# Kernel tuning notes

Measured on AMD Instinct MI355X. Metric: run time of the kernel, lower is better.

## Reference

```python
import jax, jax.numpy as jnp
import numpy as np

NUM_HEADS = 8
ROPE_BASE = 10000.0


def _rope(x):
    # x: [b, n, c]; RoPE with channel_dims=(n,), feature_dim=c, k_max=c//2
    b, n, c = x.shape
    k_max = c // 2
    theta = 1.0 / (ROPE_BASE ** (jnp.arange(k_max, dtype=jnp.float32) / k_max))
    angles = jnp.arange(n, dtype=jnp.float32)[:, None] * theta  # [n, k_max]
    cos = jnp.cos(angles)
    sin = jnp.sin(angles)
    xr = x[..., 0::2]  # real parts  [b, n, k_max]
    xi = x[..., 1::2]  # imag parts
    pr = cos * xr - sin * xi
    pi = cos * xi + sin * xr
    # original concatenates real half then imag half (no re-interleave)
    return jnp.concatenate([pr, pi], axis=-1)


def setup_inputs() -> dict:
    key = jax.random.key(0)
    ks = jax.random.split(key, 5)
    b, n, c = 4, 4096, 1024
    x = jax.random.normal(ks[0], (b, n, c), dtype=jnp.float32)
    qk_w = jax.random.normal(ks[1], (c, 2 * c), dtype=jnp.float32) * (1.0 / np.sqrt(c))
    qk_b = jnp.zeros((2 * c,), dtype=jnp.float32)
    lepe_w = jax.random.normal(ks[2], (3, c, c), dtype=jnp.float32) * (1.0 / np.sqrt(3 * c))  # [W, I, O]
    lepe_b = jnp.zeros((c,), dtype=jnp.float32)
    return {"x": x, "qk_w": qk_w, "qk_b": qk_b, "lepe_w": lepe_w, "lepe_b": lepe_b}


def reference(x, qk_w, qk_b, lepe_w, lepe_b):
    b, n, c = x.shape
    h = NUM_HEADS
    d = c // h

    qk = x @ qk_w + qk_b
    q, k = jnp.split(qk, 2, axis=-1)
    q = jax.nn.elu(q) + 1.0
    k = jax.nn.elu(k) + 1.0

    q_rope = _rope(q)
    k_rope = _rope(k)

    def to_heads(t):  # [b, n, c] -> [b, h, n, d]
        return t.reshape(b, n, h, d).transpose(0, 2, 1, 3)

    qh = to_heads(q)
    kh = to_heads(k)
    qr = to_heads(q_rope)
    kr = to_heads(k_rope)
    vh = to_heads(x)

    # z = 1 / (q . mean_n(k) + eps)  -> [b, h, n, 1]
    k_mean = jnp.mean(kh, axis=2, keepdims=True)  # [b, h, 1, d]
    z = 1.0 / (jnp.einsum('bhnd,bhmd->bhnm', qh, k_mean) + 1e-6)

    # kv = k_rope^T v / sqrt(n)  -> [b, h, d, d]
    kv = jnp.einsum('bhnd,bhne->bhde', kr, vh) * (1.0 / jnp.sqrt(jnp.float32(n)))
    out = jnp.einsum('bhnd,bhde->bhne', qr, kv) * z  # [b, h, n, d]

    out = out.transpose(0, 2, 1, 3).reshape(b, n, c)

    # lepe: Conv1D(dim, 3, padding='same') applied to v (== original x)
    lepe = jax.lax.conv_general_dilated(
        x, lepe_w, window_strides=(1,), padding='SAME',
        dimension_numbers=('NWC', 'WIO', 'NWC')) + lepe_b
    return out + lepe
```

## Files before the change

kernel.cpp:

```cpp
#include <hip/hip_runtime.h>
#include <cmath>

#define BB 4
#define NN 4096
#define CC 1024
#define HH 8
#define DD 128
#define MM (BB*NN)
#define NP (NN+2)

typedef __attribute__((ext_vector_type(8))) short bf16x8;
typedef __attribute__((ext_vector_type(4))) float f32x4;

static __device__ __forceinline__ unsigned short f2bf(float f) {
    unsigned int u = __float_as_uint(f);
    unsigned int r = (u + 0x7FFF + ((u >> 16) & 1)) >> 16;
    return (unsigned short)r;
}
static __device__ __forceinline__ float bf2f(short s) {
    return __uint_as_float(((unsigned int)(unsigned short)s) << 16);
}
static __device__ __forceinline__ float4 bf4(ushort4 u) {
    float4 f;
    f.x = __uint_as_float((unsigned int)u.x << 16);
    f.y = __uint_as_float((unsigned int)u.y << 16);
    f.z = __uint_as_float((unsigned int)u.z << 16);
    f.w = __uint_as_float((unsigned int)u.w << 16);
    return f;
}

static __device__ __forceinline__ void load_lds16(const void* g, void* l) {
    __builtin_amdgcn_global_load_lds(
        (const __attribute__((address_space(1))) unsigned int*)g,
        (__attribute__((address_space(3))) unsigned int*)l, 16, 0, 0);
}

static __device__ __forceinline__ int swz(int row, int ko) {
    return (row * 64 + ko) ^ ((row & 7) << 3);
}

#define CFENCE() asm volatile("" ::: "memory")
#define BAR() do { CFENCE(); __builtin_amdgcn_s_barrier(); CFENCE(); } while (0)

__global__ __launch_bounds__(256) void padx_kernel(
    const float* __restrict__ x, unsigned short* __restrict__ xpad)
{
    const int r = blockIdx.x;
    const int b = r / NP, p = r % NP;
    const int c = threadIdx.x * 4;
    ushort4 v = {0, 0, 0, 0};
    if (p >= 1 && p <= NN) {
        const float4 f = *(const float4*)&x[(size_t)(b * NN + p - 1) * CC + c];
        v.x = f2bf(f.x); v.y = f2bf(f.y); v.z = f2bf(f.z); v.w = f2bf(f.w);
    }
    *(ushort4*)&xpad[(size_t)r * CC + c] = v;
}

__global__ __launch_bounds__(256) void transpose_bf16_kernel(
    const float* __restrict__ src, unsigned short* __restrict__ dst,
    int R, int Cc)
{
    __shared__ float t[32][33];
    const int r0 = blockIdx.y * 32, c0 = blockIdx.x * 32;
    const int tx = threadIdx.x & 31, ty = threadIdx.x >> 5;
    #pragma unroll
    for (int i = 0; i < 4; ++i) {
        int r = ty + i * 8;
        t[r][tx] = src[(size_t)(r0 + r) * Cc + c0 + tx];
    }
    __syncthreads();
    #pragma unroll
    for (int i = 0; i < 4; ++i) {
        int r = ty + i * 8;
        dst[(size_t)(c0 + r) * R + r0 + tx] = f2bf(t[tx][r]);
    }
}

static __device__ __forceinline__ void stage_half(
    const unsigned short* __restrict__ g, int stride,
    unsigned short* lds, int tid)
{
    const int wb = tid & ~63;
    #pragma unroll
    for (int l = 0; l < 2; ++l) {
        const int c = l * 512 + tid;
        const int row = c >> 3;
        const int col8 = (c & 7) ^ (row & 7);
        load_lds16(&g[(size_t)row * stride + col8 * 8],
                   &lds[(size_t)(l * 512 + wb) * 8]);
    }
}

static __device__ __forceinline__ void lda4(
    const unsigned short* __restrict__ h, int lr0, int rl, int ko, bf16x8* o)
{
    #pragma unroll
    for (int i = 0; i < 4; ++i)
        o[i] = *(const bf16x8*)&h[swz(lr0 + i * 16 + rl, ko)];
}

static __device__ __forceinline__ void mfma_quad(
    f32x4 (*acc)[4], int mfb, const bf16x8* af, const bf16x8* bfr)
{
    __builtin_amdgcn_s_setprio(1);
    #pragma unroll
    for (int i = 0; i < 4; ++i)
        #pragma unroll
        for (int nf = 0; nf < 4; ++nf)
            acc[mfb + i][nf] = __builtin_amdgcn_mfma_f32_16x16x32_bf16(
                af[i], bfr[nf], acc[mfb + i][nf], 0, 0, 0);
    __builtin_amdgcn_s_setprio(0);
}

#define KTILE_4PHASE(Ah, Bh, blr0, STAGE_A0, STAGE_A1, STAGE_B0, STAGE_B1, HAVE_NEXT) \
    do {                                                                     \
        bf16x8 af_[4], af2_[4], bfr_[4], bfr2_[4];                           \
                                                                \
        if (HAVE_NEXT) {                                                     \
            STAGE_A0;                                                        \
            asm volatile("s_waitcnt vmcnt(2)" ::: "memory");                 \
        } else {                                                             \
            asm volatile("s_waitcnt vmcnt(0)" ::: "memory");                 \
        }                                                                    \
        BAR();                                                               \
        lda4(Ah, 0, rl, ko0, af_);                                           \
        lda4(Bh, blr0, rl, ko0, bfr_);                                       \
        mfma_quad(acc, 0, af_, bfr_);                                        \
        BAR();                                                               \
                                                                \
        lda4(Ah, 64, rl, ko0, af2_);                                         \
        if (HAVE_NEXT) { STAGE_A1; }                                         \
        BAR();                                                               \
        mfma_quad(acc, 4, af2_, bfr_);                                       \
        BAR();                                                               \
                                                                \
        lda4(Ah, 0, rl, ko1, af_);                                           \
        lda4(Bh, blr0, rl, ko1, bfr2_);                                      \
        if (HAVE_NEXT) { STAGE_B0; }                                         \
        BAR();                                                               \
        mfma_quad(acc, 0, af_, bfr2_);                                       \
        BAR();                                                               \
                                                                \
        lda4(Ah, 64, rl, ko1, af2_);                                         \
        if (HAVE_NEXT) { STAGE_B1; }                                         \
        BAR();                                                               \
        mfma_quad(acc, 4, af2_, bfr2_);                                      \
        BAR();                                                               \
    } while (0)

__global__ __launch_bounds__(512) void gemm_qk_mfma(
    const unsigned short* __restrict__ xpad, const unsigned short* __restrict__ wT,
    const float* __restrict__ bias, unsigned short* __restrict__ qbuf,
    unsigned short* __restrict__ kbuf, float* __restrict__ ksum)
{
    __shared__ __align__(16) unsigned short SA[2][2][8192];
    __shared__ __align__(16) unsigned short SB[2][2][8192];
    const int m0 = blockIdx.x * 256;
    const int n0 = blockIdx.y * 256;
    const int tid = threadIdx.x;
    const int lane = tid & 63;
    const int wv = tid >> 6;
    const int wr = wv >> 2, wc = wv & 3;
    const int b = m0 >> 12;
    const int rbase = m0 + 1 + 2 * b;
    const int rl = lane & 15;
    const int ko0 = (lane >> 4) * 8;
    const int ko1 = 32 + ko0;
    const int blr0 = (wc & 1) * 64;

    const unsigned short* Agl = &xpad[(size_t)rbase * CC];
    const unsigned short* Bgl = &wT[(size_t)n0 * CC];

    f32x4 acc[8][4] = {};
    stage_half(Agl, CC, SA[0][0], tid);
    stage_half(&Agl[(size_t)128 * CC], CC, SA[0][1], tid);
    stage_half(Bgl, CC, SB[0][0], tid);
    stage_half(&Bgl[(size_t)128 * CC], CC, SB[0][1], tid);

    const int NT = 16;
    for (int t = 0; t < NT; ++t) {
        const int cur = t & 1;
        const unsigned short* Ah = SA[cur][wr];
        const unsigned short* Bh = SB[cur][wc >> 1];
        const int k1 = (t + 1) * 64;
        KTILE_4PHASE(Ah, Bh, blr0,
            stage_half(&Agl[k1], CC, SA[cur ^ 1][0], tid),
            stage_half(&Agl[(size_t)128 * CC + k1], CC, SA[cur ^ 1][1], tid),
            stage_half(&Bgl[k1], CC, SB[cur ^ 1][0], tid),
            stage_half(&Bgl[(size_t)128 * CC + k1], CC, SB[cur ^ 1][1], tid),
            (t + 1 < NT));
    }

    const bool khalf = (n0 >= CC);
    const int col = lane & 15, rb4 = (lane >> 4) * 4;
    #pragma unroll
    for (int nf = 0; nf < 4; ++nf) {
        const int n = n0 + wc * 64 + nf * 16 + col;
        const float bn = bias[n];
        float csum = 0.0f;
        #pragma unroll
        for (int mf = 0; mf < 8; ++mf)
            #pragma unroll
            for (int r = 0; r < 4; ++r) {
                const int m = m0 + wr * 128 + mf * 16 + rb4 + r;
                float v = acc[mf][nf][r] + bn;
                v = (v > 0.0f) ? (v + 1.0f) : __expf(v);
                csum += v;
                if (!khalf) qbuf[(size_t)m * CC + n] = f2bf(v);
                else        kbuf[(size_t)m * CC + (n - CC)] = f2bf(v);
            }
        if (khalf) atomicAdd(&ksum[b * CC + (n - CC)], csum);
    }
}

__global__ __launch_bounds__(256) void rope_z_kernel(
    unsigned short* __restrict__ qbuf, const unsigned short* __restrict__ kbuf,
    const float* __restrict__ ksum, unsigned short* __restrict__ krP,
    float* __restrict__ zbuf)
{
    const int tid = threadIdx.x;
    const int row = tid >> 3;
    const int h = tid & 7;
    const int m = blockIdx.x * 32 + row;
    const int b = m >> 12;
    const int pos = m & (NN - 1);
    unsigned short* qrow = qbuf + (size_t)m * CC + h * DD;
    const unsigned short* krow = kbuf + (size_t)m * CC + h * DD;

    bf16x8 qv[16], kv8[16];
    #pragma unroll
    for (int i = 0; i < 16; ++i) {
        qv[i]  = *(const bf16x8*)&qrow[i * 8];
        kv8[i] = *(const bf16x8*)&krow[i * 8];
    }
    const float* km = ksum + b * CC + h * DD;
    float dot = 0.0f;
    #pragma unroll
    for (int i = 0; i < 16; ++i)
        #pragma unroll
        for (int jq = 0; jq < 8; ++jq)
            dot = fmaf(bf2f(qv[i][jq]), km[i * 8 + jq], dot);
    dot *= (1.0f / (float)NN);
    __syncthreads();
    zbuf[(size_t)m * HH + h] = 1.0f / (dot + 1e-6f);

    #pragma unroll
    for (int c8 = 0; c8 < 8; ++c8) {
        bf16x8 qpr, qpi, kpr, kpi;
        #pragma unroll
        for (int u = 0; u < 8; ++u) {
            const int jj = c8 * 8 + u;
            const int j = h * 64 + jj;
            const float theta = __builtin_exp2f((float)j * (-13.287712379549449f / 512.0f));
            float sv, cv;
            __sincosf((float)pos * theta, &sv, &cv);
            const int li = c8 * 2 + (u >> 2);
            const int le = (2 * u) & 7;
            const float q0 = bf2f(qv[li][le]),  q1 = bf2f(qv[li][le + 1]);
            const float k0 = bf2f(kv8[li][le]), k1 = bf2f(kv8[li][le + 1]);
            qpr[u] = (short)f2bf(cv * q0 - sv * q1);
            qpi[u] = (short)f2bf(cv * q1 + sv * q0);
            kpr[u] = (short)f2bf(cv * k0 - sv * k1);
            kpi[u] = (short)f2bf(cv * k1 + sv * k0);
        }
        *(bf16x8*)&qbuf[(size_t)m * CC + h * 64 + c8 * 8] = qpr;
        *(bf16x8*)&qbuf[(size_t)m * CC + 512 + h * 64 + c8 * 8] = qpi;
        unsigned short* kp1 = &krP[((size_t)(b * 8 + (h >> 1)) * NN + pos) * DD + (h & 1) * 64 + c8 * 8];
        unsigned short* kp2 = &krP[((size_t)(b * 8 + 4 + (h >> 1)) * NN + pos) * DD + (h & 1) * 64 + c8 * 8];
        *(bf16x8*)kp1 = kpr;
        *(bf16x8*)kp2 = kpi;
    }
}

__global__ __launch_bounds__(256) void kv_kernel(
    const unsigned short* __restrict__ krP, const unsigned short* __restrict__ xpad,
    float* __restrict__ kvpart)
{
    __shared__ float ksm[8][132];
    __shared__ float vsm[8][132];
    const int bh = blockIdx.x;
    const int slice = blockIdx.y;
    const int b = bh >> 3, h = bh & 7;
    const int n0 = slice * 256;
    const int tid = threadIdx.x;
    const int td = (tid >> 4) * 8;
    const int te = (tid & 15) * 8;
    const unsigned short* kp = krP + ((size_t)bh * NN + n0) * DD;
    const unsigned short* vp = xpad + ((size_t)(b * NP) + 1 + n0) * CC + h * DD;
    const int sr = tid >> 5;
    const int sc = (tid & 31) * 4;
    float acc[8][8] = {};
    ushort4 kq = *(const ushort4*)&kp[(size_t)sr * DD + sc];
    ushort4 vq = *(const ushort4*)&vp[(size_t)sr * CC + sc];
    for (int r0 = 0; r0 < 256; r0 += 8) {
        *(float4*)&ksm[sr][sc] = bf4(kq);
        *(float4*)&vsm[sr][sc] = bf4(vq);
        __syncthreads();
        if (r0 + 8 < 256) {
            kq = *(const ushort4*)&kp[(size_t)(r0 + 8 + sr) * DD + sc];
            vq = *(const ushort4*)&vp[(size_t)(r0 + 8 + sr) * CC + sc];
        }
        #pragma unroll
        for (int r = 0; r < 8; ++r) {
            float a[8], bv[8];
            *(float4*)&a[0]  = *(const float4*)&ksm[r][td];
            *(float4*)&a[4]  = *(const float4*)&ksm[r][td + 4];
            *(float4*)&bv[0] = *(const float4*)&vsm[r][te];
            *(float4*)&bv[4] = *(const float4*)&vsm[r][te + 4];
            #pragma unroll
            for (int i = 0; i < 8; ++i)
                #pragma unroll
                for (int j = 0; j < 8; ++j)
                    acc[i][j] = fmaf(a[i], bv[j], acc[i][j]);
        }
        __syncthreads();
    }
    float* op = kvpart + ((size_t)slice * 32 + bh) * (DD * DD);
    #pragma unroll
    for (int i = 0; i < 8; ++i)
        #pragma unroll
        for (int j = 0; j < 8; j += 4)
            *(float4*)&op[(td + i) * DD + te + j] = *(float4*)&acc[i][j];
}

__global__ __launch_bounds__(256) void kv_reduce_t_kernel(
    const float* __restrict__ kvpart, unsigned short* __restrict__ kvT)
{
    __shared__ float t[32][33];
    const int bh = blockIdx.y;
    const int dblk = blockIdx.x >> 2, eblk = blockIdx.x & 3;
    const int tx = threadIdx.x & 31, ty = threadIdx.x >> 5;
    #pragma unroll
    for (int i = 0; i < 4; ++i) {
        const int d = dblk * 32 + ty + i * 8;
        float s = 0.0f;
        #pragma unroll
        for (int sl = 0; sl < 16; ++sl)
            s += kvpart[((size_t)sl * 32 + bh) * (DD * DD) + (size_t)d * DD + eblk * 32 + tx];
        t[ty + i * 8][tx] = s * (1.0f / 64.0f);
    }
    __syncthreads();
    #pragma unroll
    for (int i = 0; i < 4; ++i) {
        const int e = ty + i * 8;
        kvT[((size_t)bh * DD + eblk * 32 + e) * DD + dblk * 32 + tx] = f2bf(t[tx][e]);
    }
}

__global__ __launch_bounds__(512) void lepe_mfma(
    const unsigned short* __restrict__ xpad, const unsigned short* __restrict__ wT,
    const float* __restrict__ bias, const unsigned short* __restrict__ qr,
    const unsigned short* __restrict__ kvT, const float* __restrict__ z,
    float* __restrict__ out)
{
    __shared__ __align__(16) unsigned short SA[2][2][8192];
    __shared__ __align__(16) unsigned short SB[2][2][8192];
    const int m0 = blockIdx.x * 256;
    const int n0 = blockIdx.y * 256;
    const int tid = threadIdx.x;
    const int lane = tid & 63;
    const int wv = tid >> 6;
    const int wr = wv >> 2, wc = wv & 3;
    const int b = m0 >> 12;
    const int rbase = m0 + 1 + 2 * b;
    const int rl = lane & 15;
    const int ko0 = (lane >> 4) * 8;
    const int ko1 = 32 + ko0;
    const int blr0 = (wc & 1) * 64;
    const int rb4 = (lane >> 4) * 4;
    const int h0 = n0 >> 7;
    const int hw = h0 + (wc >> 1);

    f32x4 acc[8][4] = {};

    #pragma unroll
    for (int kt = 0; kt < 2; ++kt) {
        stage_half(&qr[(size_t)m0 * CC + h0 * DD + kt * 64], CC, SA[0][0], tid);
        stage_half(&qr[(size_t)(m0 + 128) * CC + h0 * DD + kt * 64], CC, SA[0][1], tid);
        stage_half(&qr[(size_t)m0 * CC + (h0 + 1) * DD + kt * 64], CC, SA[1][0], tid);
        stage_half(&qr[(size_t)(m0 + 128) * CC + (h0 + 1) * DD + kt * 64], CC, SA[1][1], tid);
        stage_half(&kvT[(size_t)(b * 8 + h0) * DD * DD + kt * 64], DD, SB[0][0], tid);
        stage_half(&kvT[(size_t)(b * 8 + h0) * DD * DD + (size_t)128 * DD + kt * 64], DD, SB[0][1], tid);
        __syncthreads();
        const unsigned short* Ah = SA[wc >> 1][wr];
        const unsigned short* Bh = SB[0][wc >> 1];
        bf16x8 af[4], af2[4], bfr[4], bfr2[4];
        lda4(Ah, 0, rl, ko0, af);
        lda4(Bh, blr0, rl, ko0, bfr);
        mfma_quad(acc, 0, af, bfr);
        lda4(Ah, 64, rl, ko0, af2);
        mfma_quad(acc, 4, af2, bfr);
        lda4(Ah, 0, rl, ko1, af);
        lda4(Bh, blr0, rl, ko1, bfr2);
        mfma_quad(acc, 0, af, bfr2);
        lda4(Ah, 64, rl, ko1, af2);
        mfma_quad(acc, 4, af2, bfr2);
        __syncthreads();
    }

    #pragma unroll
    for (int mf = 0; mf < 8; ++mf)
        #pragma unroll
        for (int r = 0; r < 4; ++r) {
            const float zz = z[(size_t)(m0 + wr * 128 + mf * 16 + rb4 + r) * HH + hw];
            #pragma unroll
            for (int nf = 0; nf < 4; ++nf)
                acc[mf][nf][r] *= zz;
        }
    asm volatile("s_waitcnt vmcnt(0)" ::: "memory");

    const unsigned short* Bgl = &wT[(size_t)n0 * (3 * CC)];
    {
        const unsigned short* A0 = &xpad[(size_t)(rbase - 1) * CC];
        stage_half(A0, CC, SA[0][0], tid);
        stage_half(&A0[(size_t)128 * CC], CC, SA[0][1], tid);
        stage_half(Bgl, 3 * CC, SB[0][0], tid);
        stage_half(&Bgl[(size_t)128 * (3 * CC)], 3 * CC, SB[0][1], tid);
    }
    const int NT = 48;
    for (int t = 0; t < NT; ++t) {
        const int cur = t & 1;
        const unsigned short* Ah = SA[cur][wr];
        const unsigned short* Bh = SB[cur][wc >> 1];
        const int k1 = (t + 1) * 64;
        const int sh1 = (k1 >> 10) - 1;
        const int i1 = k1 & (CC - 1);
        const unsigned short* An = &xpad[(size_t)(rbase + sh1) * CC + i1];
        KTILE_4PHASE(Ah, Bh, blr0,
            stage_half(An, CC, SA[cur ^ 1][0], tid),
            stage_half(&An[(size_t)128 * CC], CC, SA[cur ^ 1][1], tid),
            stage_half(&Bgl[k1], 3 * CC, SB[cur ^ 1][0], tid),
            stage_half(&Bgl[(size_t)128 * (3 * CC) + k1], 3 * CC, SB[cur ^ 1][1], tid),
            (t + 1 < NT));
    }

    const int col = lane & 15;
    #pragma unroll
    for (int nf = 0; nf < 4; ++nf) {
        const int n = n0 + wc * 64 + nf * 16 + col;
        const float bn = bias[n];
        #pragma unroll
        for (int mf = 0; mf < 8; ++mf)
            #pragma unroll
            for (int r = 0; r < 4; ++r) {
                const int m = m0 + wr * 128 + mf * 16 + rb4 + r;
                out[(size_t)m * CC + n] = acc[mf][nf][r] + bn;
            }
    }
}

extern "C" void kernel_launch(void* const* d_in, const int* in_sizes, int n_in,
                              void* d_out, int out_size, void* d_ws, size_t ws_size,
                              hipStream_t stream)
{
    const float* x      = (const float*)d_in[0];
    const float* qk_w   = (const float*)d_in[1];
    const float* qk_b   = (const float*)d_in[2];
    const float* lepe_w = (const float*)d_in[3];
    const float* lepe_b = (const float*)d_in[4];
    float* out = (float*)d_out;

    float* ws     = (float*)d_ws;
    float* zbuf   = ws;
    float* ksum   = zbuf + (size_t)MM * HH;
    float* kvpart = ksum + (size_t)BB * CC;
    unsigned short* xpad = (unsigned short*)(kvpart + (size_t)16 * 32 * DD * DD);
    unsigned short* wqT  = xpad + (size_t)BB * NP * CC;
    unsigned short* wlT  = wqT + (size_t)2 * CC * CC;
    unsigned short* qbuf = wlT + (size_t)CC * 3 * CC;
    unsigned short* kbuf = qbuf + (size_t)MM * CC;
    unsigned short* krP  = kbuf + (size_t)MM * CC;
    unsigned short* kvT  = krP + (size_t)32 * NN * DD;

    hipMemsetAsync(ksum, 0, BB * CC * sizeof(float), stream);

    padx_kernel          <<<BB * NP,                      256, 0, stream>>>(x, xpad);
    transpose_bf16_kernel<<<dim3(2 * CC / 32, CC / 32),   256, 0, stream>>>(qk_w, wqT, CC, 2 * CC);
    transpose_bf16_kernel<<<dim3(CC / 32, 3 * CC / 32),   256, 0, stream>>>(lepe_w, wlT, 3 * CC, CC);

    gemm_qk_mfma      <<<dim3(MM / 256, 2048 / 256), 512, 0, stream>>>(xpad, wqT, qk_b, qbuf, kbuf, ksum);
    rope_z_kernel     <<<MM / 32,                    256, 0, stream>>>(qbuf, kbuf, ksum, krP, zbuf);
    kv_kernel         <<<dim3(32, 16),               256, 0, stream>>>(krP, xpad, kvpart);
    kv_reduce_t_kernel<<<dim3(16, 32),               256, 0, stream>>>(kvpart, kvT);
    lepe_mfma         <<<dim3(MM / 256, CC / 256),   512, 0, stream>>>(xpad, wlT, lepe_b, qbuf, kvT, zbuf, out);
}
```

Before: 521.0 us.

## Fuse RoPE into QK GEMM epilogue and simplify k-tile MFMA schedule

Applies the RoPE rotation in the QK GEMM epilogue, using a lane shuffle to fetch the paired element. Rotated q goes to a new buffer and rotated k goes straight to the permuted krP layout, so rope_z_kernel shrinks to a z-only kernel and no longer reads and rewrites q and k. The k-tile loop also replaces the four-phase barrier schedule with one staging step followed by a single mfma_ktile call, cutting barriers per tile. The costs are strided scalar bf16 stores and a sincos per element in the epilogue, plus less overlap between global staging and MFMA work.

```diff
diff --git a/kernel.cpp b/kernel.cpp
--- a/kernel.cpp
+++ b/kernel.cpp
@@ -112,10 +112,31 @@
     __builtin_amdgcn_s_setprio(0);
 }
 
+static __device__ __forceinline__ void mfma_ktile(
+    const unsigned short* __restrict__ Ah, const unsigned short* __restrict__ Bh,
+    int blr0, int rl, int kq, f32x4 acc[8][4])
+{
+    __builtin_amdgcn_s_setprio(1);
+    #pragma unroll
+    for (int ks = 0; ks < 2; ++ks) {
+        const int ko = ks * 32 + kq;
+        bf16x8 af[8], bfr[4];
+        lda4(Ah, 0, rl, ko, af);
+        lda4(Ah, 64, rl, ko, af + 4);
+        lda4(Bh, blr0, rl, ko, bfr);
+        #pragma unroll
+        for (int mf = 0; mf < 8; ++mf)
+            #pragma unroll
+            for (int nf = 0; nf < 4; ++nf)
+                acc[mf][nf] = __builtin_amdgcn_mfma_f32_16x16x32_bf16(
+                    af[mf], bfr[nf], acc[mf][nf], 0, 0, 0);
+    }
+    __builtin_amdgcn_s_setprio(0);
+}
+
 #define KTILE_4PHASE(Ah, Bh, blr0, STAGE_A0, STAGE_A1, STAGE_B0, STAGE_B1, HAVE_NEXT) \
     do {                                                                     \
         bf16x8 af_[4], af2_[4], bfr_[4], bfr2_[4];                           \
-                                                                \
         if (HAVE_NEXT) {                                                     \
             STAGE_A0;                                                        \
             asm volatile("s_waitcnt vmcnt(2)" ::: "memory");                 \
@@ -127,20 +148,17 @@
         lda4(Bh, blr0, rl, ko0, bfr_);                                       \
         mfma_quad(acc, 0, af_, bfr_);                                        \
         BAR();                                                               \
-                                                                \
         lda4(Ah, 64, rl, ko0, af2_);                                         \
         if (HAVE_NEXT) { STAGE_A1; }                                         \
         BAR();                                                               \
         mfma_quad(acc, 4, af2_, bfr_);                                       \
         BAR();                                                               \
-                                                                \
         lda4(Ah, 0, rl, ko1, af_);                                           \
         lda4(Bh, blr0, rl, ko1, bfr2_);                                      \
         if (HAVE_NEXT) { STAGE_B0; }                                         \
         BAR();                                                               \
         mfma_quad(acc, 0, af_, bfr2_);                                       \
         BAR();                                                               \
-                                                                \
         lda4(Ah, 64, rl, ko1, af2_);                                         \
         if (HAVE_NEXT) { STAGE_B1; }                                         \
         BAR();                                                               \
@@ -151,7 +169,8 @@
 __global__ __launch_bounds__(512) void gemm_qk_mfma(
     const unsigned short* __restrict__ xpad, const unsigned short* __restrict__ wT,
     const float* __restrict__ bias, unsigned short* __restrict__ qbuf,
-    unsigned short* __restrict__ kbuf, float* __restrict__ ksum)
+    unsigned short* __restrict__ qrbuf, unsigned short* __restrict__ krP,
+    float* __restrict__ ksum)
 {
     __shared__ __align__(16) unsigned short SA[2][2][8192];
     __shared__ __align__(16) unsigned short SB[2][2][8192];
@@ -164,8 +183,7 @@
     const int b = m0 >> 12;
     const int rbase = m0 + 1 + 2 * b;
     const int rl = lane & 15;
-    const int ko0 = (lane >> 4) * 8;
-    const int ko1 = 32 + ko0;
+    const int kq = (lane >> 4) * 8;
     const int blr0 = (wc & 1) * 64;
 
     const unsigned short* Agl = &xpad[(size_t)rbase * CC];
@@ -180,15 +198,19 @@
     const int NT = 16;
     for (int t = 0; t < NT; ++t) {
         const int cur = t & 1;
-        const unsigned short* Ah = SA[cur][wr];
-        const unsigned short* Bh = SB[cur][wc >> 1];
-        const int k1 = (t + 1) * 64;
-        KTILE_4PHASE(Ah, Bh, blr0,
-            stage_half(&Agl[k1], CC, SA[cur ^ 1][0], tid),
-            stage_half(&Agl[(size_t)128 * CC + k1], CC, SA[cur ^ 1][1], tid),
-            stage_half(&Bgl[k1], CC, SB[cur ^ 1][0], tid),
-            stage_half(&Bgl[(size_t)128 * CC + k1], CC, SB[cur ^ 1][1], tid),
-            (t + 1 < NT));
+        if (t + 1 < NT) {
+            const int k1 = (t + 1) * 64;
+            stage_half(&Agl[k1], CC, SA[cur ^ 1][0], tid);
+            stage_half(&Agl[(size_t)128 * CC + k1], CC, SA[cur ^ 1][1], tid);
+            stage_half(&Bgl[k1], CC, SB[cur ^ 1][0], tid);
+            stage_half(&Bgl[(size_t)128 * CC + k1], CC, SB[cur ^ 1][1], tid);
+            asm volatile("s_waitcnt vmcnt(8)" ::: "memory");
+        } else {
+            asm volatile("s_waitcnt vmcnt(0)" ::: "memory");
+        }
+        BAR();
+        mfma_ktile(SA[cur][wr], SB[cur][wc >> 1], blr0, rl, kq, acc);
+        BAR();
     }
 
     const bool khalf = (n0 >= CC);
@@ -197,6 +219,9 @@
     for (int nf = 0; nf < 4; ++nf) {
         const int n = n0 + wc * 64 + nf * 16 + col;
         const float bn = bias[n];
+        const int jpair = (khalf ? (n - CC) : n) >> 1;
+        const float theta = __builtin_exp2f((float)jpair * (-13.287712379549449f / 512.0f));
+        const bool odd = (n & 1) != 0;
         float csum = 0.0f;
         #pragma unroll
         for (int mf = 0; mf < 8; ++mf)
@@ -206,16 +231,28 @@
                 float v = acc[mf][nf][r] + bn;
                 v = (v > 0.0f) ? (v + 1.0f) : __expf(v);
                 csum += v;
-                if (!khalf) qbuf[(size_t)m * CC + n] = f2bf(v);
-                else        kbuf[(size_t)m * CC + (n - CC)] = f2bf(v);
+                const float p = __shfl_xor(v, 1);
+                float sv, cv;
+                __sincosf((float)(m & (NN - 1)) * theta, &sv, &cv);
+                const float rot = odd ? (cv * v + sv * p) : (cv * v - sv * p);
+                if (!khalf) {
+                    qbuf[(size_t)m * CC + n] = f2bf(v);
+                    const int qcol = odd ? (512 + jpair) : jpair;
+                    qrbuf[(size_t)m * CC + qcol] = f2bf(rot);
+                } else {
+                    const int kc = n - CC;
+                    const int h = kc >> 7;
+                    const int jj = jpair & 63;
+                    krP[((size_t)(b * 8 + (odd ? 4 : 0) + (h >> 1)) * NN + (m & (NN - 1))) * DD
+                        + (h & 1) * 64 + jj] = f2bf(rot);
+                }
             }
         if (khalf) atomicAdd(&ksum[b * CC + (n - CC)], csum);
     }
 }
 
-__global__ __launch_bounds__(256) void rope_z_kernel(
-    unsigned short* __restrict__ qbuf, const unsigned short* __restrict__ kbuf,
-    const float* __restrict__ ksum, unsigned short* __restrict__ krP,
+__global__ __launch_bounds__(256) void z_kernel(
+    const unsigned short* __restrict__ qbuf, const float* __restrict__ ksum,
     float* __restrict__ zbuf)
 {
     const int tid = threadIdx.x;
@@ -223,53 +260,18 @@
     const int h = tid & 7;
     const int m = blockIdx.x * 32 + row;
     const int b = m >> 12;
-    const int pos = m & (NN - 1);
-    unsigned short* qrow = qbuf + (size_t)m * CC + h * DD;
-    const unsigned short* krow = kbuf + (size_t)m * CC + h * DD;
-
-    bf16x8 qv[16], kv8[16];
-    #pragma unroll
-    for (int i = 0; i < 16; ++i) {
-        qv[i]  = *(const bf16x8*)&qrow[i * 8];
-        kv8[i] = *(const bf16x8*)&krow[i * 8];
-    }
+    const unsigned short* qrow = qbuf + (size_t)m * CC + h * DD;
     const float* km = ksum + b * CC + h * DD;
     float dot = 0.0f;
     #pragma unroll
-    for (int i = 0; i < 16; ++i)
+    for (int i = 0; i < 16; ++i) {
+        const bf16x8 qv = *(const bf16x8*)&qrow[i * 8];
         #pragma unroll
         for (int jq = 0; jq < 8; ++jq)
-            dot = fmaf(bf2f(qv[i][jq]), km[i * 8 + jq], dot);
+            dot = fmaf(bf2f(qv[jq]), km[i * 8 + jq], dot);
+    }
     dot *= (1.0f / (float)NN);
-    __syncthreads();
     zbuf[(size_t)m * HH + h] = 1.0f / (dot + 1e-6f);
-
-    #pragma unroll
-    for (int c8 = 0; c8 < 8; ++c8) {
-        bf16x8 qpr, qpi, kpr, kpi;
-        #pragma unroll
-        for (int u = 0; u < 8; ++u) {
-            const int jj = c8 * 8 + u;
-            const int j = h * 64 + jj;
-            const float theta = __builtin_exp2f((float)j * (-13.287712379549449f / 512.0f));
-            float sv, cv;
-            __sincosf((float)pos * theta, &sv, &cv);
-            const int li = c8 * 2 + (u >> 2);
-            const int le = (2 * u) & 7;
-            const float q0 = bf2f(qv[li][le]),  q1 = bf2f(qv[li][le + 1]);
-            const float k0 = bf2f(kv8[li][le]), k1 = bf2f(kv8[li][le + 1]);
-            qpr[u] = (short)f2bf(cv * q0 - sv * q1);
-            qpi[u] = (short)f2bf(cv * q1 + sv * q0);
-            kpr[u] = (short)f2bf(cv * k0 - sv * k1);
-            kpi[u] = (short)f2bf(cv * k1 + sv * k0);
-        }
-        *(bf16x8*)&qbuf[(size_t)m * CC + h * 64 + c8 * 8] = qpr;
-        *(bf16x8*)&qbuf[(size_t)m * CC + 512 + h * 64 + c8 * 8] = qpi;
-        unsigned short* kp1 = &krP[((size_t)(b * 8 + (h >> 1)) * NN + pos) * DD + (h & 1) * 64 + c8 * 8];
-        unsigned short* kp2 = &krP[((size_t)(b * 8 + 4 + (h >> 1)) * NN + pos) * DD + (h & 1) * 64 + c8 * 8];
-        *(bf16x8*)kp1 = kpr;
-        *(bf16x8*)kp2 = kpi;
-    }
 }
 
 __global__ __launch_bounds__(256) void kv_kernel(
@@ -382,19 +384,7 @@
         stage_half(&kvT[(size_t)(b * 8 + h0) * DD * DD + kt * 64], DD, SB[0][0], tid);
         stage_half(&kvT[(size_t)(b * 8 + h0) * DD * DD + (size_t)128 * DD + kt * 64], DD, SB[0][1], tid);
         __syncthreads();
-        const unsigned short* Ah = SA[wc >> 1][wr];
-        const unsigned short* Bh = SB[0][wc >> 1];
-        bf16x8 af[4], af2[4], bfr[4], bfr2[4];
-        lda4(Ah, 0, rl, ko0, af);
-        lda4(Bh, blr0, rl, ko0, bfr);
-        mfma_quad(acc, 0, af, bfr);
-        lda4(Ah, 64, rl, ko0, af2);
-        mfma_quad(acc, 4, af2, bfr);
-        lda4(Ah, 0, rl, ko1, af);
-        lda4(Bh, blr0, rl, ko1, bfr2);
-        mfma_quad(acc, 0, af, bfr2);
-        lda4(Ah, 64, rl, ko1, af2);
-        mfma_quad(acc, 4, af2, bfr2);
+        mfma_ktile(SA[wc >> 1][wr], SB[0][wc >> 1], blr0, rl, ko0, acc);
         __syncthreads();
     }
 
@@ -464,13 +454,13 @@
     float* zbuf   = ws;
     float* ksum   = zbuf + (size_t)MM * HH;
     float* kvpart = ksum + (size_t)BB * CC;
-    unsigned short* xpad = (unsigned short*)(kvpart + (size_t)16 * 32 * DD * DD);
-    unsigned short* wqT  = xpad + (size_t)BB * NP * CC;
-    unsigned short* wlT  = wqT + (size_t)2 * CC * CC;
-    unsigned short* qbuf = wlT + (size_t)CC * 3 * CC;
-    unsigned short* kbuf = qbuf + (size_t)MM * CC;
-    unsigned short* krP  = kbuf + (size_t)MM * CC;
-    unsigned short* kvT  = krP + (size_t)32 * NN * DD;
+    unsigned short* xpad  = (unsigned short*)(kvpart + (size_t)16 * 32 * DD * DD);
+    unsigned short* wqT   = xpad + (size_t)BB * NP * CC;
+    unsigned short* wlT   = wqT + (size_t)2 * CC * CC;
+    unsigned short* qbuf  = wlT + (size_t)CC * 3 * CC;
+    unsigned short* qrbuf = qbuf + (size_t)MM * CC;
+    unsigned short* krP   = qrbuf + (size_t)MM * CC;
+    unsigned short* kvT   = krP + (size_t)32 * NN * DD;
 
     hipMemsetAsync(ksum, 0, BB * CC * sizeof(float), stream);
 
@@ -478,9 +468,9 @@
     transpose_bf16_kernel<<<dim3(2 * CC / 32, CC / 32),   256, 0, stream>>>(qk_w, wqT, CC, 2 * CC);
     transpose_bf16_kernel<<<dim3(CC / 32, 3 * CC / 32),   256, 0, stream>>>(lepe_w, wlT, 3 * CC, CC);
 
-    gemm_qk_mfma      <<<dim3(MM / 256, 2048 / 256), 512, 0, stream>>>(xpad, wqT, qk_b, qbuf, kbuf, ksum);
-    rope_z_kernel     <<<MM / 32,                    256, 0, stream>>>(qbuf, kbuf, ksum, krP, zbuf);
+    gemm_qk_mfma      <<<dim3(MM / 256, 2048 / 256), 512, 0, stream>>>(xpad, wqT, qk_b, qbuf, qrbuf, krP, ksum);
+    z_kernel          <<<MM / 32,                    256, 0, stream>>>(qbuf, ksum, zbuf);
     kv_kernel         <<<dim3(32, 16),               256, 0, stream>>>(krP, xpad, kvpart);
     kv_reduce_t_kernel<<<dim3(16, 32),               256, 0, stream>>>(kvpart, kvT);
-    lepe_mfma         <<<dim3(MM / 256, CC / 256),   512, 0, stream>>>(xpad, wlT, lepe_b, qbuf, kvT, zbuf, out);
-}
+    lepe_mfma         <<<dim3(MM / 256, CC / 256),   512, 0, stream>>>(xpad, wlT, lepe_b, qrbuf, kvT, zbuf, out);
+}
```

Result: faster. 488.4 us (-6.3%).
